# Kernel optimization log

Measured on AMD Instinct MI355X. Metric: run time of the kernel, lower is better.

## Reference

```python
import jax, jax.numpy as jnp
import numpy as np

DIM = 512
N = 1024
DIM_HEAD = 64
HEADS = 8
BATCH = 8
SCALE = DIM_HEAD ** -0.5


def setup_inputs() -> dict:
    key = jax.random.key(0)
    ks = jax.random.split(key, 9)
    s = 0.02
    return {
        "x": jax.random.normal(ks[0], (BATCH, N, DIM), dtype=jnp.float32),
        "w_qkv": jax.random.normal(ks[1], (3 * DIM, DIM), dtype=jnp.float32) * s,
        "b_qkv": jax.random.normal(ks[2], (3 * DIM,), dtype=jnp.float32) * s,
        "wq": jax.random.normal(ks[3], (N, DIM_HEAD), dtype=jnp.float32) * s,
        "bq": jax.random.normal(ks[4], (N,), dtype=jnp.float32) * s,
        "wk": jax.random.normal(ks[5], (N, DIM_HEAD), dtype=jnp.float32) * s,
        "bk": jax.random.normal(ks[6], (N,), dtype=jnp.float32) * s,
        "w_out": jax.random.normal(ks[7], (DIM, DIM), dtype=jnp.float32) * s,
        "b_out": jax.random.normal(ks[8], (DIM,), dtype=jnp.float32) * s,
    }


def _split_heads(t):
    # [b, n, h*d] -> [b, h, n, d]
    b, n, _ = t.shape
    return t.reshape(b, n, HEADS, DIM_HEAD).transpose(0, 2, 1, 3)


def reference(x, w_qkv, b_qkv, wq, bq, wk, bk, w_out, b_out):
    # fused QKV projection: [b, n, 3*dim]
    qkv = x @ w_qkv.T + b_qkv
    qo, ko, vo = jnp.split(qkv, 3, axis=-1)
    q, k, v = _split_heads(qo), _split_heads(ko), _split_heads(vo)  # [b,h,n,d]

    # additive-attention stage 1: A = softmax(Wq(q) * scale) over last dim
    A = jax.nn.softmax((jnp.einsum('bhnd,md->bhnm', q, wq) + bq) * SCALE, axis=-1)  # [b,h,n,n]
    q_global = jnp.sum(jnp.einsum('bhnm,bhmd->bhnd', A, q), axis=-1, keepdims=True)  # [b,h,n,1]
    p = q_global * k  # [b,h,n,d]

    # stage 2
    B = jax.nn.softmax((jnp.einsum('bhnd,md->bhnm', p, wk) + bk) * SCALE, axis=-1)  # [b,h,n,n]
    k_global = jnp.sum(jnp.einsum('bhnm,bhmd->bhnd', B, p), axis=-1, keepdims=True)  # [b,h,n,1]

    u = (k_global * v).transpose(0, 2, 1, 3).reshape(x.shape[0], N, DIM)  # [b,n,dim]
    out = u @ w_out.T + b_out + qo
    return out
```

## Files before the change

kernel.cpp:

```cpp
#include <hip/hip_runtime.h>


#define SCL 0.125f
typedef unsigned short u16;
typedef __attribute__((ext_vector_type(8))) short short8;
typedef __attribute__((ext_vector_type(4))) float f32x4;

#define MFMA16(a, b, c) __builtin_amdgcn_mfma_f32_16x16x32_bf16((a), (b), (c), 0, 0, 0)

__device__ __forceinline__ float bf2f(u16 u) {
    union { unsigned int i; float f; } v; v.i = ((unsigned int)u) << 16; return v.f;
}
__device__ __forceinline__ u16 f2bf(float f) {
    union { float f; unsigned int i; } v; v.f = f;
    unsigned int x = v.i;
    return (u16)((x + 0x7FFFu + ((x >> 16) & 1u)) >> 16);
}

__global__ __launch_bounds__(256) void conv_kernel(
    const float* __restrict__ w_qkv, const float* __restrict__ w_out,
    const float* __restrict__ wq, const float* __restrict__ wk,
    const float* __restrict__ x, u16* __restrict__ wsb)
{
    const int idx = (blockIdx.x * 256 + threadIdx.x) * 4;
    const float* src; int off;
    if      (idx < 786432)  { src = w_qkv; off = idx; }
    else if (idx < 1048576) { src = w_out; off = idx - 786432; }
    else if (idx < 1114112) { src = wq;    off = idx - 1048576; }
    else if (idx < 1179648) { src = wk;    off = idx - 1114112; }
    else                    { src = x;     off = idx - 1179648; }
    float4 v = *(const float4*)(src + off);
    ushort4 o; o.x = f2bf(v.x); o.y = f2bf(v.y); o.z = f2bf(v.z); o.w = f2bf(v.w);
    *(ushort4*)(wsb + idx) = o;
}

#define MQK 0
#define MVU 1
#define MOUT 2

template <int MODE>
__global__ __launch_bounds__(256) void gemm_k(
    const u16* __restrict__ Ab, int lda, int acol,
    const u16* __restrict__ Wb, const float* __restrict__ bias,
    const float* __restrict__ kg, const u16* __restrict__ qkws_ro,
    u16* __restrict__ qkws, float* __restrict__ outp)
{
    __shared__ u16 As[128 * 72];
    __shared__ u16 Bs[64 * 72];
    const int t = threadIdx.x;
    const int w = t >> 6, lane = t & 63, s = lane & 15, quad = lane >> 4;
    const int bm = blockIdx.x * 128, jn0 = blockIdx.y * 64;

    f32x4 acc[2][4];
#pragma unroll
    for (int i = 0; i < 2; ++i)
#pragma unroll
        for (int j = 0; j < 4; ++j) acc[i][j] = (f32x4){0.f, 0.f, 0.f, 0.f};

    for (int kt = 0; kt < 512; kt += 64) {
        __syncthreads();
        {
            const int row = t >> 1, ch = (t & 1) * 32;
            const u16* sp = Ab + (size_t)(bm + row) * lda + acol + kt + ch;
#pragma unroll
            for (int i = 0; i < 4; ++i)
                *(uint4*)&As[row * 72 + ch + i * 8] = *(const uint4*)(sp + i * 8);
            const int r = t >> 2, bch = (t & 3) * 16;
            const u16* bp = Wb + (size_t)(jn0 + r) * 512 + kt + bch;
            *(uint4*)&Bs[r * 72 + bch]     = *(const uint4*)bp;
            *(uint4*)&Bs[r * 72 + bch + 8] = *(const uint4*)(bp + 8);
        }
        __syncthreads();
#pragma unroll
        for (int kk = 0; kk < 2; ++kk) {
            short8 a0 = *(const short8*)&As[(w * 32 + s) * 72 + kk * 32 + quad * 8];
            short8 a1 = *(const short8*)&As[(w * 32 + 16 + s) * 72 + kk * 32 + quad * 8];
#pragma unroll
            for (int ct = 0; ct < 4; ++ct) {
                short8 bf = *(const short8*)&Bs[(ct * 16 + s) * 72 + kk * 32 + quad * 8];
                acc[0][ct] = MFMA16(a0, bf, acc[0][ct]);
                acc[1][ct] = MFMA16(a1, bf, acc[1][ct]);
            }
        }
    }

    if constexpr (MODE == MOUT) {
#pragma unroll
        for (int mt = 0; mt < 2; ++mt)
#pragma unroll
            for (int ct = 0; ct < 4; ++ct) {
                const int jn = jn0 + ct * 16 + s;
#pragma unroll
                for (int r = 0; r < 4; ++r) {
                    const int row = bm + w * 32 + mt * 16 + quad * 4 + r;
                    outp[(size_t)row * 512 + jn] =
                        acc[mt][ct][r] + bias[jn] + bf2f(qkws_ro[(size_t)row * 1024 + jn]);
                }
            }
    } else {
        __syncthreads();
#pragma unroll
        for (int mt = 0; mt < 2; ++mt)
#pragma unroll
            for (int ct = 0; ct < 4; ++ct) {
                const int jn = jn0 + ct * 16 + s;
#pragma unroll
                for (int r = 0; r < 4; ++r) {
                    const int rowl = w * 32 + mt * 16 + quad * 4 + r;
                    float v = acc[mt][ct][r] + bias[jn];
                    if constexpr (MODE == MVU) {
                        const int row = bm + rowl;
                        v *= kg[(((row >> 10) * 8 + (jn >> 6)) << 10) | (row & 1023)];
                    }
                    As[rowl * 72 + ct * 16 + s] = f2bf(v);
                }
            }
        __syncthreads();
        const int row = t >> 1, ch = (t & 1) * 32;
        u16* dp = qkws + (size_t)(bm + row) * 1024 + (MODE == MVU ? 512 : 0) + jn0 + ch;
#pragma unroll
        for (int i = 0; i < 4; ++i)
            *(uint4*)(dp + i * 8) = *(const uint4*)&As[row * 72 + ch + i * 8];
    }
}

__global__ __launch_bounds__(256) void qsks_kernel(
    const u16* __restrict__ qkws, float* __restrict__ qs, float* __restrict__ ks)
{
    const int tid = blockIdx.x * 256 + threadIdx.x;
    const int n = tid & 1023, bh = tid >> 10, b = bh >> 3, h = bh & 7;
    const u16* base = qkws + (size_t)((b << 10) + n) * 1024 + (h << 6);
    float sq = 0.f, sk = 0.f;
#pragma unroll
    for (int i = 0; i < 64; i += 8) {
        union { uint4 q; u16 u[8]; } a, c;
        a.q = *(const uint4*)(base + i);
        c.q = *(const uint4*)(base + 512 + i);
#pragma unroll
        for (int j = 0; j < 8; ++j) { sq += bf2f(a.u[j]); sk += bf2f(c.u[j]); }
    }
    qs[tid] = sq; ks[tid] = sk;
}

__global__ __launch_bounds__(256) void stage_soft(
    const u16* __restrict__ qkws, int qcol0,
    const u16* __restrict__ wmb, const float* __restrict__ biasv,
    const float* __restrict__ rowscale,
    const float* __restrict__ wv1, const float* __restrict__ wv2,
    float* __restrict__ outg)
{
    __shared__ float zr[4][64], wr[4][64];
    const int t = threadIdx.x;
    const int w = t >> 6, lane = t & 63, s = lane & 15, quad = lane >> 4;
    const int n0 = blockIdx.x * 64;
    const int bh = blockIdx.y, b = bh >> 3, h = bh & 7;

    short8 qa[4][2];
#pragma unroll
    for (int nt = 0; nt < 4; ++nt)
#pragma unroll
        for (int kk = 0; kk < 2; ++kk)
            qa[nt][kk] = *(const short8*)&qkws[
                (size_t)((b << 10) + n0 + nt * 16 + s) * 1024 + qcol0 + (h << 6) + kk * 32 + quad * 8];

    float rs[4][4];
#pragma unroll
    for (int nt = 0; nt < 4; ++nt)
#pragma unroll
        for (int r = 0; r < 4; ++r)
            rs[nt][r] = rowscale ? rowscale[(bh << 10) + n0 + nt * 16 + quad * 4 + r] : 1.0f;

    float z[4][4] = {}, wa[4][4] = {};

    for (int mi = 0; mi < 16; ++mi) {
        const int mt = w * 256 + mi * 16;
        const u16* bp = wmb + (size_t)(mt + s) * 64 + quad * 8;
        short8 bf0 = *(const short8*)bp;
        short8 bf1 = *(const short8*)(bp + 32);
        const float bm = biasv[mt + s];
        float wv = wv1[(bh << 10) + mt + s];
        if (wv2) wv *= wv2[(bh << 10) + mt + s];
#pragma unroll
        for (int nt = 0; nt < 4; ++nt) {
            f32x4 a = (f32x4){0.f, 0.f, 0.f, 0.f};
            a = MFMA16(qa[nt][0], bf0, a);
            a = MFMA16(qa[nt][1], bf1, a);
#pragma unroll
            for (int r = 0; r < 4; ++r) {
                const float l = (rs[nt][r] * a[r] + bm) * SCL;
                const float e = __expf(l);
                z[nt][r] += e;
                wa[nt][r] += e * wv;
            }
        }
    }

#pragma unroll
    for (int nt = 0; nt < 4; ++nt)
#pragma unroll
        for (int r = 0; r < 4; ++r) {
            float Z = z[nt][r], W = wa[nt][r];
            for (int off = 1; off < 16; off <<= 1) {
                Z += __shfl_xor(Z, off);
                W += __shfl_xor(W, off);
            }
            if (s == 0) {
                zr[w][nt * 16 + quad * 4 + r] = Z;
                wr[w][nt * 16 + quad * 4 + r] = W;
            }
        }
    __syncthreads();
    if (t < 64) {
        float Z = zr[0][t] + zr[1][t] + zr[2][t] + zr[3][t];
        float W = wr[0][t] + wr[1][t] + wr[2][t] + wr[3][t];
        outg[(bh << 10) + n0 + t] = W / Z;
    }
}

extern "C" void kernel_launch(void* const* d_in, const int* in_sizes, int n_in,
                              void* d_out, int out_size, void* d_ws, size_t ws_size,
                              hipStream_t stream)
{
    const float* x     = (const float*)d_in[0];
    const float* w_qkv = (const float*)d_in[1];
    const float* b_qkv = (const float*)d_in[2];
    const float* wq    = (const float*)d_in[3];
    const float* bq    = (const float*)d_in[4];
    const float* wk    = (const float*)d_in[5];
    const float* bk    = (const float*)d_in[6];
    const float* w_out = (const float*)d_in[7];
    const float* b_out = (const float*)d_in[8];
    float* out = (float*)d_out;

    float* qs = (float*)d_ws;
    float* ks = qs + 65536;
    float* qg = ks + 65536;
    float* kg = qg + 65536;
    u16* wsb   = (u16*)(kg + 65536);
    u16* wqkvb = wsb;
    u16* woutb = wqkvb + 786432;
    u16* wqb   = woutb + 262144;
    u16* wkb   = wqb + 65536;
    u16* xb    = wkb + 65536;
    u16* qkws  = xb + 4194304;

    conv_kernel<<<5248, 256, 0, stream>>>(w_qkv, w_out, wq, wk, x, wsb);
    gemm_k<MQK><<<dim3(64, 16), 256, 0, stream>>>(
        xb, 512, 0, wqkvb, b_qkv, nullptr, nullptr, qkws, nullptr);
    qsks_kernel<<<256, 256, 0, stream>>>(qkws, qs, ks);
    stage_soft<<<dim3(16, 64), 256, 0, stream>>>(
        qkws, 0, wqb, bq, nullptr, qs, nullptr, qg);
    stage_soft<<<dim3(16, 64), 256, 0, stream>>>(
        qkws, 512, wkb, bk, qg, qg, ks, kg);
    gemm_k<MVU><<<dim3(64, 8), 256, 0, stream>>>(
        xb, 512, 0, wqkvb + (size_t)1024 * 512, b_qkv + 1024, kg, nullptr, qkws, nullptr);
    gemm_k<MOUT><<<dim3(64, 8), 256, 0, stream>>>(
        qkws, 1024, 512, woutb, b_out, nullptr, qkws, nullptr, out);
}
```

Baseline: 189.9 us.

## Fuse QKV GEMM with row sums and apply kg scaling in stage two

The QKV projection becomes a single 128x128-tiled GEMM that writes all of Q, K and V into a 1536-wide workspace and computes the per-head q/k row sums in its epilogue. This removes the separate qsks kernel and the second V GEMM. The second softmax stage now scales V by k_global and writes u in place over the K columns, which the output GEMM reads directly. Larger tiles with a K-step of 32 change the register and LDS footprint, and the grid for the QKV and output GEMMs gets smaller.

New measurement: 194.0 us. +2.1%, slower.

```diff
diff --git a/kernel.cpp b/kernel.cpp
--- a/kernel.cpp
+++ b/kernel.cpp
@@ -15,6 +15,12 @@
     union { float f; unsigned int i; } v; v.f = f;
     unsigned int x = v.i;
     return (u16)((x + 0x7FFFu + ((x >> 16) & 1u)) >> 16);
+}
+__device__ __forceinline__ uint4 pack8(const float* v) {
+    union { u16 u[8]; uint4 q; } r;
+#pragma unroll
+    for (int i = 0; i < 8; ++i) r.u[i] = f2bf(v[i]);
+    return r.q;
 }
 
 __global__ __launch_bounds__(256) void conv_kernel(
@@ -34,122 +40,127 @@
     *(ushort4*)(wsb + idx) = o;
 }
 
-#define MQK 0
-#define MVU 1
-#define MOUT 2
+#define MQKV 0
+#define MOUT 1
 
 template <int MODE>
-__global__ __launch_bounds__(256) void gemm_k(
+__global__ __launch_bounds__(256) void gemm128(
     const u16* __restrict__ Ab, int lda, int acol,
-    const u16* __restrict__ Wb, const float* __restrict__ bias,
-    const float* __restrict__ kg, const u16* __restrict__ qkws_ro,
-    u16* __restrict__ qkws, float* __restrict__ outp)
-{
-    __shared__ u16 As[128 * 72];
-    __shared__ u16 Bs[64 * 72];
+    const u16* __restrict__ Wb, int ldb,
+    const float* __restrict__ biasf,
+    const u16* __restrict__ qkro,
+    float* __restrict__ qsv, float* __restrict__ ksv,
+    u16* __restrict__ Cws, float* __restrict__ outp)
+{
+    __shared__ u16 S[8192];
+    u16* As = S;
+    u16* Bs = S + 4096;
+
     const int t = threadIdx.x;
     const int w = t >> 6, lane = t & 63, s = lane & 15, quad = lane >> 4;
-    const int bm = blockIdx.x * 128, jn0 = blockIdx.y * 64;
-
-    f32x4 acc[2][4];
-#pragma unroll
-    for (int i = 0; i < 2; ++i)
+    const int wr = w >> 1, wc = w & 1;
+    const int bm = blockIdx.x * 128, jn0 = blockIdx.y * 128;
+    const int arow = t >> 1, ac0 = (t & 1) * 16;
+
+    f32x4 acc[4][4];
+#pragma unroll
+    for (int i = 0; i < 4; ++i)
 #pragma unroll
         for (int j = 0; j < 4; ++j) acc[i][j] = (f32x4){0.f, 0.f, 0.f, 0.f};
 
-    for (int kt = 0; kt < 512; kt += 64) {
+    for (int kt = 0; kt < 512; kt += 32) {
         __syncthreads();
         {
-            const int row = t >> 1, ch = (t & 1) * 32;
-            const u16* sp = Ab + (size_t)(bm + row) * lda + acol + kt + ch;
+            const u16* ap = Ab + (size_t)(bm + arow) * lda + acol + kt + ac0;
+            *(uint4*)&As[arow * 32 + ac0]     = *(const uint4*)ap;
+            *(uint4*)&As[arow * 32 + ac0 + 8] = *(const uint4*)(ap + 8);
+            const u16* bp = Wb + (size_t)(jn0 + arow) * ldb + kt + ac0;
+            *(uint4*)&Bs[arow * 32 + ac0]     = *(const uint4*)bp;
+            *(uint4*)&Bs[arow * 32 + ac0 + 8] = *(const uint4*)(bp + 8);
+        }
+        __syncthreads();
+        short8 af[4], bf[4];
+#pragma unroll
+        for (int mt = 0; mt < 4; ++mt)
+            af[mt] = *(const short8*)&As[(wr * 64 + mt * 16 + s) * 32 + quad * 8];
+#pragma unroll
+        for (int ct = 0; ct < 4; ++ct)
+            bf[ct] = *(const short8*)&Bs[(wc * 64 + ct * 16 + s) * 32 + quad * 8];
+#pragma unroll
+        for (int mt = 0; mt < 4; ++mt)
+#pragma unroll
+            for (int ct = 0; ct < 4; ++ct)
+                acc[mt][ct] = MFMA16(af[mt], bf[ct], acc[mt][ct]);
+    }
+
+    float bb[4];
+#pragma unroll
+    for (int ct = 0; ct < 4; ++ct) bb[ct] = biasf[jn0 + wc * 64 + ct * 16 + s];
+
+    if constexpr (MODE == MOUT) {
+#pragma unroll
+        for (int mt = 0; mt < 4; ++mt)
+#pragma unroll
+            for (int ct = 0; ct < 4; ++ct) {
+                const int col = jn0 + wc * 64 + ct * 16 + s;
+#pragma unroll
+                for (int r = 0; r < 4; ++r) {
+                    const int row = bm + wr * 64 + mt * 16 + quad * 4 + r;
+                    outp[(size_t)row * 512 + col] =
+                        acc[mt][ct][r] + bb[ct] + bf2f(qkro[(size_t)row * 1536 + col]);
+                }
+            }
+    } else {
+        const int c0 = jn0 + wc * 64;
+        if (c0 < 1024) {
+            const int h = (c0 & 511) >> 6;
+            float* dst = (c0 < 512) ? qsv : ksv;
+#pragma unroll
+            for (int mt = 0; mt < 4; ++mt)
+#pragma unroll
+                for (int r = 0; r < 4; ++r) {
+                    float v = (acc[mt][0][r] + bb[0]) + (acc[mt][1][r] + bb[1]) +
+                              (acc[mt][2][r] + bb[2]) + (acc[mt][3][r] + bb[3]);
+                    v += __shfl_xor(v, 1); v += __shfl_xor(v, 2);
+                    v += __shfl_xor(v, 4); v += __shfl_xor(v, 8);
+                    if (s == 0) {
+                        const int row = bm + wr * 64 + mt * 16 + quad * 4 + r;
+                        dst[((((row >> 10) << 3) + h) << 10) | (row & 1023)] = v;
+                    }
+                }
+        }
+#pragma unroll
+        for (int half = 0; half < 2; ++half) {
+            __syncthreads();
+            if (wr == half) {
+#pragma unroll
+                for (int mt = 0; mt < 4; ++mt)
+#pragma unroll
+                    for (int ct = 0; ct < 4; ++ct)
+#pragma unroll
+                        for (int r = 0; r < 4; ++r)
+                            S[(mt * 16 + quad * 4 + r) * 128 + wc * 64 + ct * 16 + s] =
+                                f2bf(acc[mt][ct][r] + bb[ct]);
+            }
+            __syncthreads();
+            const int row = t >> 2, coff = (t & 3) * 32;
+            u16* dp = Cws + (size_t)(bm + half * 64 + row) * 1536 + jn0 + coff;
 #pragma unroll
             for (int i = 0; i < 4; ++i)
-                *(uint4*)&As[row * 72 + ch + i * 8] = *(const uint4*)(sp + i * 8);
-            const int r = t >> 2, bch = (t & 3) * 16;
-            const u16* bp = Wb + (size_t)(jn0 + r) * 512 + kt + bch;
-            *(uint4*)&Bs[r * 72 + bch]     = *(const uint4*)bp;
-            *(uint4*)&Bs[r * 72 + bch + 8] = *(const uint4*)(bp + 8);
-        }
-        __syncthreads();
-#pragma unroll
-        for (int kk = 0; kk < 2; ++kk) {
-            short8 a0 = *(const short8*)&As[(w * 32 + s) * 72 + kk * 32 + quad * 8];
-            short8 a1 = *(const short8*)&As[(w * 32 + 16 + s) * 72 + kk * 32 + quad * 8];
-#pragma unroll
-            for (int ct = 0; ct < 4; ++ct) {
-                short8 bf = *(const short8*)&Bs[(ct * 16 + s) * 72 + kk * 32 + quad * 8];
-                acc[0][ct] = MFMA16(a0, bf, acc[0][ct]);
-                acc[1][ct] = MFMA16(a1, bf, acc[1][ct]);
-            }
-        }
-    }
-
-    if constexpr (MODE == MOUT) {
-#pragma unroll
-        for (int mt = 0; mt < 2; ++mt)
-#pragma unroll
-            for (int ct = 0; ct < 4; ++ct) {
-                const int jn = jn0 + ct * 16 + s;
-#pragma unroll
-                for (int r = 0; r < 4; ++r) {
-                    const int row = bm + w * 32 + mt * 16 + quad * 4 + r;
-                    outp[(size_t)row * 512 + jn] =
-                        acc[mt][ct][r] + bias[jn] + bf2f(qkws_ro[(size_t)row * 1024 + jn]);
-                }
-            }
-    } else {
-        __syncthreads();
-#pragma unroll
-        for (int mt = 0; mt < 2; ++mt)
-#pragma unroll
-            for (int ct = 0; ct < 4; ++ct) {
-                const int jn = jn0 + ct * 16 + s;
-#pragma unroll
-                for (int r = 0; r < 4; ++r) {
-                    const int rowl = w * 32 + mt * 16 + quad * 4 + r;
-                    float v = acc[mt][ct][r] + bias[jn];
-                    if constexpr (MODE == MVU) {
-                        const int row = bm + rowl;
-                        v *= kg[(((row >> 10) * 8 + (jn >> 6)) << 10) | (row & 1023)];
-                    }
-                    As[rowl * 72 + ct * 16 + s] = f2bf(v);
-                }
-            }
-        __syncthreads();
-        const int row = t >> 1, ch = (t & 1) * 32;
-        u16* dp = qkws + (size_t)(bm + row) * 1024 + (MODE == MVU ? 512 : 0) + jn0 + ch;
-#pragma unroll
-        for (int i = 0; i < 4; ++i)
-            *(uint4*)(dp + i * 8) = *(const uint4*)&As[row * 72 + ch + i * 8];
-    }
-}
-
-__global__ __launch_bounds__(256) void qsks_kernel(
-    const u16* __restrict__ qkws, float* __restrict__ qs, float* __restrict__ ks)
-{
-    const int tid = blockIdx.x * 256 + threadIdx.x;
-    const int n = tid & 1023, bh = tid >> 10, b = bh >> 3, h = bh & 7;
-    const u16* base = qkws + (size_t)((b << 10) + n) * 1024 + (h << 6);
-    float sq = 0.f, sk = 0.f;
-#pragma unroll
-    for (int i = 0; i < 64; i += 8) {
-        union { uint4 q; u16 u[8]; } a, c;
-        a.q = *(const uint4*)(base + i);
-        c.q = *(const uint4*)(base + 512 + i);
-#pragma unroll
-        for (int j = 0; j < 8; ++j) { sq += bf2f(a.u[j]); sk += bf2f(c.u[j]); }
-    }
-    qs[tid] = sq; ks[tid] = sk;
-}
-
+                *(uint4*)(dp + i * 8) = *(const uint4*)&S[row * 128 + coff + i * 8];
+        }
+    }
+}
+
+template <bool DOU>
 __global__ __launch_bounds__(256) void stage_soft(
-    const u16* __restrict__ qkws, int qcol0,
+    u16* __restrict__ qkws, int qcol0,
     const u16* __restrict__ wmb, const float* __restrict__ biasv,
     const float* __restrict__ rowscale,
     const float* __restrict__ wv1, const float* __restrict__ wv2,
     float* __restrict__ outg)
 {
-    __shared__ float zr[4][64], wr[4][64];
+    __shared__ float zr[4][64], wrs[4][64], kgv[64];
     const int t = threadIdx.x;
     const int w = t >> 6, lane = t & 63, s = lane & 15, quad = lane >> 4;
     const int n0 = blockIdx.x * 64;
@@ -161,7 +172,7 @@
 #pragma unroll
         for (int kk = 0; kk < 2; ++kk)
             qa[nt][kk] = *(const short8*)&qkws[
-                (size_t)((b << 10) + n0 + nt * 16 + s) * 1024 + qcol0 + (h << 6) + kk * 32 + quad * 8];
+                (size_t)((b << 10) + n0 + nt * 16 + s) * 1536 + qcol0 + (h << 6) + kk * 32 + quad * 8];
 
     float rs[4][4];
 #pragma unroll
@@ -206,14 +217,31 @@
             }
             if (s == 0) {
                 zr[w][nt * 16 + quad * 4 + r] = Z;
-                wr[w][nt * 16 + quad * 4 + r] = W;
+                wrs[w][nt * 16 + quad * 4 + r] = W;
             }
         }
     __syncthreads();
     if (t < 64) {
-        float Z = zr[0][t] + zr[1][t] + zr[2][t] + zr[3][t];
-        float W = wr[0][t] + wr[1][t] + wr[2][t] + wr[3][t];
-        outg[(bh << 10) + n0 + t] = W / Z;
+        const float Z = zr[0][t] + zr[1][t] + zr[2][t] + zr[3][t];
+        const float W = wrs[0][t] + wrs[1][t] + wrs[2][t] + wrs[3][t];
+        const float v = W / Z;
+        outg[(bh << 10) + n0 + t] = v;
+        kgv[t] = v;
+    }
+    if constexpr (DOU) {
+        __syncthreads();
+        const int rl = t >> 2, d0 = (t & 3) * 16;
+        const float kgf = kgv[rl];
+        const size_t base = (size_t)((b << 10) + n0 + rl) * 1536 + (h << 6) + d0;
+#pragma unroll
+        for (int i = 0; i < 2; ++i) {
+            union { uint4 q; u16 u[8]; } vv;
+            vv.q = *(const uint4*)&qkws[base + 1024 + i * 8];
+            float tmp[8];
+#pragma unroll
+            for (int j = 0; j < 8; ++j) tmp[j] = bf2f(vv.u[j]) * kgf;
+            *(uint4*)&qkws[base + 512 + i * 8] = pack8(tmp);
+        }
     }
 }
 
@@ -245,15 +273,12 @@
     u16* qkws  = xb + 4194304;
 
     conv_kernel<<<5248, 256, 0, stream>>>(w_qkv, w_out, wq, wk, x, wsb);
-    gemm_k<MQK><<<dim3(64, 16), 256, 0, stream>>>(
-        xb, 512, 0, wqkvb, b_qkv, nullptr, nullptr, qkws, nullptr);
-    qsks_kernel<<<256, 256, 0, stream>>>(qkws, qs, ks);
-    stage_soft<<<dim3(16, 64), 256, 0, stream>>>(
+    gemm128<MQKV><<<dim3(64, 12), 256, 0, stream>>>(
+        xb, 512, 0, wqkvb, 512, b_qkv, nullptr, qs, ks, qkws, nullptr);
+    stage_soft<false><<<dim3(16, 64), 256, 0, stream>>>(
         qkws, 0, wqb, bq, nullptr, qs, nullptr, qg);
-    stage_soft<<<dim3(16, 64), 256, 0, stream>>>(
+    stage_soft<true><<<dim3(16, 64), 256, 0, stream>>>(
         qkws, 512, wkb, bk, qg, qg, ks, kg);
-    gemm_k<MVU><<<dim3(64, 8), 256, 0, stream>>>(
-        xb, 512, 0, wqkvb + (size_t)1024 * 512, b_qkv + 1024, kg, nullptr, qkws, nullptr);
-    gemm_k<MOUT><<<dim3(64, 8), 256, 0, stream>>>(
-        qkws, 1024, 512, woutb, b_out, nullptr, qkws, nullptr, out);
-}
+    gemm128<MOUT><<<dim3(64, 4), 256, 0, stream>>>(
+        qkws, 1536, 512, woutb, 512, b_out, qkws, nullptr, nullptr, nullptr, out);
+}
```
